# Kernel tuning notes

Hardware: AMD Instinct MI355X
Metric: run time of the kernel (lower is better)

The kernel has to match this reference:

```python
import jax, jax.numpy as jnp
import numpy as np

B = 1024            # batch
F = (16, 16, 16)    # factors (f1, f2, f3)
BOND = 32           # bond dimension
SIZE = 4096         # prod(F)


def setup_inputs() -> dict:
    key = jax.random.key(0)
    k0, k1, k2, k3 = jax.random.split(key, 4)
    x = jax.random.normal(k0, (B, SIZE), dtype=jnp.float32)
    # cores: (r_{k-1}, f_k, f_k, r_k), boundary ranks = 1, init scale 0.01 as in torch
    core0 = jax.random.normal(k1, (1, F[0], F[0], BOND), dtype=jnp.float32) * 0.01
    core1 = jax.random.normal(k2, (BOND, F[1], F[1], BOND), dtype=jnp.float32) * 0.01
    core2 = jax.random.normal(k3, (BOND, F[2], F[2], 1), dtype=jnp.float32) * 0.01
    bias = jnp.zeros((SIZE,), dtype=jnp.float32)
    return {"x": x, "core0": core0, "core1": core1, "core2": core2, "bias": bias}


def reference(x, core0, core1, core2, bias):
    # Batched MPO (tensor-train) matvec: y[b, i1 i2 i3] = sum_{j1 j2 j3, r1 r2}
    #   G0[1, i1, j1, r1] G1[r1, i2, j2, r2] G2[r2, i3, j3, 1] * x[b, j1 j2 j3]
    b = x.shape[0]
    t = x.reshape(b, F[0], F[1], F[2])                       # (B, j1, j2, j3)
    # contract j1 with core0 -> carry bond r, accumulate output index i1 at the end
    t = jnp.einsum('bjkl,aijr->brkli', t, core0)             # (B, r1, j2, j3, i1)
    # contract (r1, j2) with core1
    t = jnp.einsum('brkli,rmks->bslim', t, core1)            # (B, r2, j3, i1, i2)
    # contract (r2, j3) with core2 (right bond t has size 1)
    y = jnp.einsum('bslim,snlt->bimnt', t, core2)            # (B, i1, i2, i3, 1)
    return y.reshape(b, SIZE) + bias
```

## Files before the change

### kernel.cpp

```cpp
#include <hip/hip_runtime.h>
#include <stdint.h>

typedef float f32x4_t __attribute__((ext_vector_type(4)));
typedef __bf16 bf16x8_t __attribute__((ext_vector_type(8)));

#define GLD16(gp, lp) __builtin_amdgcn_global_load_lds( \
    (const __attribute__((address_space(1))) void*)(gp), \
    (__attribute__((address_space(3))) void*)(lp), 16, 0, 0)

__device__ __forceinline__ uint32_t f2bf(float f) {
  uint32_t u = __float_as_uint(f);
  u += 0x7FFFu + ((u >> 16) & 1u);
  return u >> 16;
}
__device__ __forceinline__ uint32_t pack2(float a, float b) {
  return f2bf(a) | (f2bf(b) << 16);
}

__global__ __launch_bounds__(256) void build_w_kernel(
    const float* __restrict__ c0, const float* __restrict__ c1,
    const float* __restrict__ c2, uint16_t* __restrict__ W) {
  __shared__ float M1[16 * 516];
  const int t = threadIdx.x;
  const int bid = blockIdx.x;
  const int i1 = bid >> 4, j1 = bid & 15;

  const float* c0b = c0 + (i1 * 16 + j1) * 32;
  const float4* c1v = (const float4*)c1;
  #pragma unroll 1
  for (int ee = 0; ee < 8; ++ee) {
    const int idx4 = t + 256 * ee;
    float ax = 0.f, ay = 0.f, az = 0.f, aw = 0.f;
    #pragma unroll 8
    for (int r1 = 0; r1 < 32; ++r1) {
      const float g = c0b[r1];
      const float4 v = c1v[r1 * 2048 + idx4];
      ax += g * v.x; ay += g * v.y; az += g * v.z; aw += g * v.w;
    }
    const int idx = idx4 * 4;
    const int i2 = idx >> 9, j2 = (idx >> 5) & 15, r2 = idx & 31;
    float* p = &M1[i2 * 516 + j2 * 32 + r2];
    p[0] = ax; p[1] = ay; p[2] = az; p[3] = aw;
  }
  __syncthreads();

  const int i2 = t >> 4, i3 = t & 15;
  const int irow = (i1 * 16 + i2) * 16 + i3;
  uint16_t* Wr = W + (size_t)irow * 4096 + j1 * 256;
  const float4* c2v = (const float4*)c2;
  const float* M1b = &M1[i2 * 516];

  #pragma unroll 1
  for (int half = 0; half < 2; ++half) {
    float acc[8][16];
    #pragma unroll
    for (int a = 0; a < 8; ++a)
      #pragma unroll
      for (int b = 0; b < 16; ++b) acc[a][b] = 0.f;

    const float* M1h = M1b + half * 8 * 32;
    #pragma unroll 4
    for (int r2 = 0; r2 < 32; ++r2) {
      const float4 q0 = c2v[r2 * 64 + i3 * 4 + 0];
      const float4 q1 = c2v[r2 * 64 + i3 * 4 + 1];
      const float4 q2 = c2v[r2 * 64 + i3 * 4 + 2];
      const float4 q3 = c2v[r2 * 64 + i3 * 4 + 3];
      float gv[16] = {q0.x, q0.y, q0.z, q0.w, q1.x, q1.y, q1.z, q1.w,
                      q2.x, q2.y, q2.z, q2.w, q3.x, q3.y, q3.z, q3.w};
      float m1v[8];
      #pragma unroll
      for (int jj = 0; jj < 8; ++jj) m1v[jj] = M1h[jj * 32 + r2];
      #pragma unroll
      for (int jj = 0; jj < 8; ++jj)
        #pragma unroll
        for (int j3 = 0; j3 < 16; ++j3)
          acc[jj][j3] += m1v[jj] * gv[j3];
    }
    #pragma unroll
    for (int jj = 0; jj < 8; ++jj) {
      uint4 o0, o1;
      o0.x = pack2(acc[jj][0],  acc[jj][1]);  o0.y = pack2(acc[jj][2],  acc[jj][3]);
      o0.z = pack2(acc[jj][4],  acc[jj][5]);  o0.w = pack2(acc[jj][6],  acc[jj][7]);
      o1.x = pack2(acc[jj][8],  acc[jj][9]);  o1.y = pack2(acc[jj][10], acc[jj][11]);
      o1.z = pack2(acc[jj][12], acc[jj][13]); o1.w = pack2(acc[jj][14], acc[jj][15]);
      uint4* dst = (uint4*)(Wr + half * 128 + jj * 16);
      dst[0] = o0; dst[1] = o1;
    }
  }
}

__global__ __launch_bounds__(256) void cvt_x_kernel(const float* __restrict__ x,
                                                    uint32_t* __restrict__ xb) {
  const int i = blockIdx.x * 256 + threadIdx.x;
  const float4* x4 = (const float4*)x;
  const float4 a = x4[2 * i], b = x4[2 * i + 1];
  uint4 o;
  o.x = pack2(a.x, a.y); o.y = pack2(a.z, a.w);
  o.z = pack2(b.x, b.y); o.w = pack2(b.z, b.w);
  ((uint4*)xb)[i] = o;
}

__global__ __launch_bounds__(256, 2) void gemm_bt_bias_kernel(
    const uint16_t* __restrict__ A, const uint16_t* __restrict__ Bt,
    const float* __restrict__ bias, float* __restrict__ C) {
  constexpr int Kd = 4096, Nd = 4096;
  __shared__ uint16_t As[64 * 64];
  __shared__ uint16_t Bs[128 * 64];
  const int t = threadIdx.x;
  const int wid = t >> 6, lane = t & 63;

  const int bid = blockIdx.x;
  const int g = bid & 7, idx = bid >> 3;
  const int ntile = g * 4 + (idx >> 4);
  const int mtile = idx & 15;
  const int brow = mtile * 64, bcol = ntile * 128;

  const uint16_t* Ab = A + (size_t)brow * Kd;
  const uint16_t* Bb = Bt + (size_t)bcol * Kd;

  const int rb = t >> 3;
  const int ce = ((t & 7) * 8) ^ ((rb & 7) << 3);
  const uint16_t* gA = Ab + (size_t)rb * Kd + ce;
  const uint16_t* gB = Bb + (size_t)rb * Kd + ce;
  uint16_t* lA0 = As + wid * 512;
  uint16_t* lA1 = As + 2048 + wid * 512;
  uint16_t* lB0 = Bs + wid * 512;
  uint16_t* lB1 = Bs + 2048 + wid * 512;
  uint16_t* lB2 = Bs + 4096 + wid * 512;
  uint16_t* lB3 = Bs + 6144 + wid * 512;

  const int wm = wid >> 1, wn = wid & 1;
  const int fr = lane & 15, fk = (lane >> 4) * 8;
  const int csw = (fr & 7) << 3;

  f32x4_t zero = {0.f, 0.f, 0.f, 0.f};
  f32x4_t acc[2][4];
  #pragma unroll
  for (int m = 0; m < 2; ++m)
    #pragma unroll
    for (int n = 0; n < 4; ++n) acc[m][n] = zero;

  for (int kt = 0; kt < Kd; kt += 64) {
    GLD16(gA + kt, lA0);
    GLD16(gA + (size_t)32 * Kd + kt, lA1);
    GLD16(gB + kt, lB0);
    GLD16(gB + (size_t)32 * Kd + kt, lB1);
    GLD16(gB + (size_t)64 * Kd + kt, lB2);
    GLD16(gB + (size_t)96 * Kd + kt, lB3);
    __syncthreads();

    bf16x8_t af[2][2], bfr[2][4];
    #pragma unroll
    for (int kk = 0; kk < 2; ++kk) {
      const int col = (kk * 32 + fk) ^ csw;
      #pragma unroll
      for (int m = 0; m < 2; ++m)
        af[kk][m] = *(const bf16x8_t*)(As + (wm * 32 + m * 16 + fr) * 64 + col);
      #pragma unroll
      for (int n = 0; n < 4; ++n)
        bfr[kk][n] = *(const bf16x8_t*)(Bs + (wn * 64 + n * 16 + fr) * 64 + col);
    }
    #pragma unroll
    for (int kk = 0; kk < 2; ++kk)
      #pragma unroll
      for (int m = 0; m < 2; ++m)
        #pragma unroll
        for (int n = 0; n < 4; ++n)
          acc[m][n] = __builtin_amdgcn_mfma_f32_16x16x32_bf16(
              af[kk][m], bfr[kk][n], acc[m][n], 0, 0, 0);
    __syncthreads();
  }

  const int orow = brow + wm * 32 + (lane >> 4) * 4;
  const int ocol = bcol + wn * 64 + fr;
  #pragma unroll
  for (int n = 0; n < 4; ++n) {
    const float bv = bias[ocol + n * 16];
    #pragma unroll
    for (int m = 0; m < 2; ++m) {
      float* Cp = C + (size_t)(orow + m * 16) * Nd + ocol + n * 16;
      #pragma unroll
      for (int r = 0; r < 4; ++r) Cp[(size_t)r * Nd] = acc[m][n][r] + bv;
    }
  }
}

extern "C" void kernel_launch(void* const* d_in, const int* in_sizes, int n_in,
                              void* d_out, int out_size, void* d_ws, size_t ws_size,
                              hipStream_t stream) {
  const float* x    = (const float*)d_in[0];
  const float* c0   = (const float*)d_in[1];
  const float* c1   = (const float*)d_in[2];
  const float* c2   = (const float*)d_in[3];
  const float* bias = (const float*)d_in[4];
  float* y = (float*)d_out;

  uint16_t* W  = (uint16_t*)d_ws;
  uint16_t* xb = (uint16_t*)d_ws + (size_t)4096 * 4096;

  build_w_kernel<<<256, 256, 0, stream>>>(c0, c1, c2, W);
  cvt_x_kernel<<<2048, 256, 0, stream>>>(x, (uint32_t*)xb);
  gemm_bt_bias_kernel<<<512, 256, 0, stream>>>(xb, W, bias, y);
}
```

Measured before the change: 169.9 us.

## Split W construction into two kernels and double-buffer GEMM LDS tiles

The dense W build is split into two stages: one kernel forms the core0·core1 product into an fp32 scratch buffer, and a second, much wider grid contracts it with core2 into bf16 W. This is meant to raise parallelism over the old 256-block kernel, which held a large per-thread accumulator. The GEMM now double-buffers its LDS tiles so the next K-slice load is issued before the current MFMAs, leaving one barrier per iteration. In exchange it doubles LDS use and adds an extra scratch round-trip, with the scratch region reused for xb after build_w2 finishes.

```diff
diff --git a/kernel.cpp b/kernel.cpp
--- a/kernel.cpp
+++ b/kernel.cpp
@@ -17,76 +17,78 @@
   return f2bf(a) | (f2bf(b) << 16);
 }
 
-__global__ __launch_bounds__(256) void build_w_kernel(
+__global__ __launch_bounds__(256) void build_m01_kernel(
     const float* __restrict__ c0, const float* __restrict__ c1,
-    const float* __restrict__ c2, uint16_t* __restrict__ W) {
-  __shared__ float M1[16 * 516];
-  const int t = threadIdx.x;
+    float* __restrict__ M01) {
+  const int a = blockIdx.x, t = threadIdx.x;
+  const int i1 = a >> 4, i2 = a & 15, j1 = t >> 4, j2 = t & 15;
+  const float* c0p = c0 + (i1 * 16 + j1) * 32;
+  const float4* c1v = (const float4*)(c1 + i2 * 512 + j2 * 32);
+
+  float acc[32];
+  #pragma unroll
+  for (int r2 = 0; r2 < 32; ++r2) acc[r2] = 0.f;
+
+  #pragma unroll 4
+  for (int r1 = 0; r1 < 32; ++r1) {
+    const float g = c0p[r1];
+    #pragma unroll
+    for (int q = 0; q < 8; ++q) {
+      const float4 v = c1v[r1 * 2048 + q];
+      acc[q * 4 + 0] += g * v.x; acc[q * 4 + 1] += g * v.y;
+      acc[q * 4 + 2] += g * v.z; acc[q * 4 + 3] += g * v.w;
+    }
+  }
+  float4* dst = (float4*)(M01 + (size_t)a * 8192 + t * 32);
+  #pragma unroll
+  for (int q = 0; q < 8; ++q) {
+    float4 v = {acc[q * 4 + 0], acc[q * 4 + 1], acc[q * 4 + 2], acc[q * 4 + 3]};
+    dst[q] = v;
+  }
+}
+
+__global__ __launch_bounds__(256) void build_w2_kernel(
+    const float* __restrict__ M01, const float* __restrict__ c2,
+    uint16_t* __restrict__ W) {
+  __shared__ float C2L[32 * 16];
   const int bid = blockIdx.x;
-  const int i1 = bid >> 4, j1 = bid & 15;
-
-  const float* c0b = c0 + (i1 * 16 + j1) * 32;
-  const float4* c1v = (const float4*)c1;
-  #pragma unroll 1
-  for (int ee = 0; ee < 8; ++ee) {
-    const int idx4 = t + 256 * ee;
-    float ax = 0.f, ay = 0.f, az = 0.f, aw = 0.f;
-    #pragma unroll 8
-    for (int r1 = 0; r1 < 32; ++r1) {
-      const float g = c0b[r1];
-      const float4 v = c1v[r1 * 2048 + idx4];
-      ax += g * v.x; ay += g * v.y; az += g * v.z; aw += g * v.w;
-    }
-    const int idx = idx4 * 4;
-    const int i2 = idx >> 9, j2 = (idx >> 5) & 15, r2 = idx & 31;
-    float* p = &M1[i2 * 516 + j2 * 32 + r2];
-    p[0] = ax; p[1] = ay; p[2] = az; p[3] = aw;
+  const int a = bid >> 4, i3 = bid & 15, t = threadIdx.x;
+
+  if (t < 128) {
+    ((float4*)C2L)[t] = ((const float4*)c2)[(t >> 2) * 64 + i3 * 4 + (t & 3)];
   }
   __syncthreads();
 
-  const int i2 = t >> 4, i3 = t & 15;
-  const int irow = (i1 * 16 + i2) * 16 + i3;
-  uint16_t* Wr = W + (size_t)irow * 4096 + j1 * 256;
-  const float4* c2v = (const float4*)c2;
-  const float* M1b = &M1[i2 * 516];
-
-  #pragma unroll 1
-  for (int half = 0; half < 2; ++half) {
-    float acc[8][16];
-    #pragma unroll
-    for (int a = 0; a < 8; ++a)
-      #pragma unroll
-      for (int b = 0; b < 16; ++b) acc[a][b] = 0.f;
-
-    const float* M1h = M1b + half * 8 * 32;
-    #pragma unroll 4
-    for (int r2 = 0; r2 < 32; ++r2) {
-      const float4 q0 = c2v[r2 * 64 + i3 * 4 + 0];
-      const float4 q1 = c2v[r2 * 64 + i3 * 4 + 1];
-      const float4 q2 = c2v[r2 * 64 + i3 * 4 + 2];
-      const float4 q3 = c2v[r2 * 64 + i3 * 4 + 3];
-      float gv[16] = {q0.x, q0.y, q0.z, q0.w, q1.x, q1.y, q1.z, q1.w,
-                      q2.x, q2.y, q2.z, q2.w, q3.x, q3.y, q3.z, q3.w};
-      float m1v[8];
-      #pragma unroll
-      for (int jj = 0; jj < 8; ++jj) m1v[jj] = M1h[jj * 32 + r2];
-      #pragma unroll
-      for (int jj = 0; jj < 8; ++jj)
-        #pragma unroll
-        for (int j3 = 0; j3 < 16; ++j3)
-          acc[jj][j3] += m1v[jj] * gv[j3];
-    }
-    #pragma unroll
-    for (int jj = 0; jj < 8; ++jj) {
-      uint4 o0, o1;
-      o0.x = pack2(acc[jj][0],  acc[jj][1]);  o0.y = pack2(acc[jj][2],  acc[jj][3]);
-      o0.z = pack2(acc[jj][4],  acc[jj][5]);  o0.w = pack2(acc[jj][6],  acc[jj][7]);
-      o1.x = pack2(acc[jj][8],  acc[jj][9]);  o1.y = pack2(acc[jj][10], acc[jj][11]);
-      o1.z = pack2(acc[jj][12], acc[jj][13]); o1.w = pack2(acc[jj][14], acc[jj][15]);
-      uint4* dst = (uint4*)(Wr + half * 128 + jj * 16);
-      dst[0] = o0; dst[1] = o1;
-    }
-  }
+  float M[32];
+  const float4* mp = (const float4*)(M01 + (size_t)a * 8192 + t * 32);
+  #pragma unroll
+  for (int q = 0; q < 8; ++q) {
+    const float4 v = mp[q];
+    M[q * 4 + 0] = v.x; M[q * 4 + 1] = v.y; M[q * 4 + 2] = v.z; M[q * 4 + 3] = v.w;
+  }
+
+  float acc[16];
+  #pragma unroll
+  for (int j = 0; j < 16; ++j) acc[j] = 0.f;
+
+  #pragma unroll 4
+  for (int r2 = 0; r2 < 32; ++r2) {
+    const float4* cp = (const float4*)(C2L + r2 * 16);
+    const float4 q0 = cp[0], q1 = cp[1], q2 = cp[2], q3 = cp[3];
+    const float m = M[r2];
+    acc[0]  += m * q0.x; acc[1]  += m * q0.y; acc[2]  += m * q0.z; acc[3]  += m * q0.w;
+    acc[4]  += m * q1.x; acc[5]  += m * q1.y; acc[6]  += m * q1.z; acc[7]  += m * q1.w;
+    acc[8]  += m * q2.x; acc[9]  += m * q2.y; acc[10] += m * q2.z; acc[11] += m * q2.w;
+    acc[12] += m * q3.x; acc[13] += m * q3.y; acc[14] += m * q3.z; acc[15] += m * q3.w;
+  }
+
+  uint4 o0, o1;
+  o0.x = pack2(acc[0],  acc[1]);  o0.y = pack2(acc[2],  acc[3]);
+  o0.z = pack2(acc[4],  acc[5]);  o0.w = pack2(acc[6],  acc[7]);
+  o1.x = pack2(acc[8],  acc[9]);  o1.y = pack2(acc[10], acc[11]);
+  o1.z = pack2(acc[12], acc[13]); o1.w = pack2(acc[14], acc[15]);
+  uint4* dst = (uint4*)(W + (size_t)(a * 16 + i3) * 4096 + t * 16);
+  dst[0] = o0; dst[1] = o1;
 }
 
 __global__ __launch_bounds__(256) void cvt_x_kernel(const float* __restrict__ x,
@@ -104,8 +106,8 @@
     const uint16_t* __restrict__ A, const uint16_t* __restrict__ Bt,
     const float* __restrict__ bias, float* __restrict__ C) {
   constexpr int Kd = 4096, Nd = 4096;
-  __shared__ uint16_t As[64 * 64];
-  __shared__ uint16_t Bs[128 * 64];
+  __shared__ uint16_t As[2][64 * 64];
+  __shared__ uint16_t Bs[2][128 * 64];
   const int t = threadIdx.x;
   const int wid = t >> 6, lane = t & 63;
 
@@ -122,12 +124,7 @@
   const int ce = ((t & 7) * 8) ^ ((rb & 7) << 3);
   const uint16_t* gA = Ab + (size_t)rb * Kd + ce;
   const uint16_t* gB = Bb + (size_t)rb * Kd + ce;
-  uint16_t* lA0 = As + wid * 512;
-  uint16_t* lA1 = As + 2048 + wid * 512;
-  uint16_t* lB0 = Bs + wid * 512;
-  uint16_t* lB1 = Bs + 2048 + wid * 512;
-  uint16_t* lB2 = Bs + 4096 + wid * 512;
-  uint16_t* lB3 = Bs + 6144 + wid * 512;
+  const int wofs = wid * 512;
 
   const int wm = wid >> 1, wn = wid & 1;
   const int fr = lane & 15, fk = (lane >> 4) * 8;
@@ -140,14 +137,22 @@
     #pragma unroll
     for (int n = 0; n < 4; ++n) acc[m][n] = zero;
 
+  #define STAGE(buf, kt)                                             \
+    do {                                                             \
+      GLD16(gA + (kt), As[buf] + wofs);                              \
+      GLD16(gA + (size_t)32 * Kd + (kt), As[buf] + 2048 + wofs);     \
+      GLD16(gB + (kt), Bs[buf] + wofs);                              \
+      GLD16(gB + (size_t)32 * Kd + (kt), Bs[buf] + 2048 + wofs);     \
+      GLD16(gB + (size_t)64 * Kd + (kt), Bs[buf] + 4096 + wofs);     \
+      GLD16(gB + (size_t)96 * Kd + (kt), Bs[buf] + 6144 + wofs);     \
+    } while (0)
+
+  STAGE(0, 0);
+  __syncthreads();
+
+  int cur = 0;
   for (int kt = 0; kt < Kd; kt += 64) {
-    GLD16(gA + kt, lA0);
-    GLD16(gA + (size_t)32 * Kd + kt, lA1);
-    GLD16(gB + kt, lB0);
-    GLD16(gB + (size_t)32 * Kd + kt, lB1);
-    GLD16(gB + (size_t)64 * Kd + kt, lB2);
-    GLD16(gB + (size_t)96 * Kd + kt, lB3);
-    __syncthreads();
+    if (kt + 64 < Kd) STAGE(cur ^ 1, kt + 64);
 
     bf16x8_t af[2][2], bfr[2][4];
     #pragma unroll
@@ -155,10 +160,10 @@
       const int col = (kk * 32 + fk) ^ csw;
       #pragma unroll
       for (int m = 0; m < 2; ++m)
-        af[kk][m] = *(const bf16x8_t*)(As + (wm * 32 + m * 16 + fr) * 64 + col);
+        af[kk][m] = *(const bf16x8_t*)(As[cur] + (wm * 32 + m * 16 + fr) * 64 + col);
       #pragma unroll
       for (int n = 0; n < 4; ++n)
-        bfr[kk][n] = *(const bf16x8_t*)(Bs + (wn * 64 + n * 16 + fr) * 64 + col);
+        bfr[kk][n] = *(const bf16x8_t*)(Bs[cur] + (wn * 64 + n * 16 + fr) * 64 + col);
     }
     #pragma unroll
     for (int kk = 0; kk < 2; ++kk)
@@ -168,8 +173,11 @@
         for (int n = 0; n < 4; ++n)
           acc[m][n] = __builtin_amdgcn_mfma_f32_16x16x32_bf16(
               af[kk][m], bfr[kk][n], acc[m][n], 0, 0, 0);
+
     __syncthreads();
-  }
+    cur ^= 1;
+  }
+  #undef STAGE
 
   const int orow = brow + wm * 32 + (lane >> 4) * 4;
   const int ocol = bcol + wn * 64 + fr;
@@ -195,10 +203,13 @@
   const float* bias = (const float*)d_in[4];
   float* y = (float*)d_out;
 
-  uint16_t* W  = (uint16_t*)d_ws;
-  uint16_t* xb = (uint16_t*)d_ws + (size_t)4096 * 4096;
-
-  build_w_kernel<<<256, 256, 0, stream>>>(c0, c1, c2, W);
+  uint16_t* W   = (uint16_t*)d_ws;
+  char*     slab = (char*)d_ws + (size_t)4096 * 4096 * 2;
+  float*    M01 = (float*)slab;
+  uint16_t* xb  = (uint16_t*)slab;
+
+  build_m01_kernel<<<256, 256, 0, stream>>>(c0, c1, M01);
+  build_w2_kernel<<<4096, 256, 0, stream>>>(M01, c2, W);
   cvt_x_kernel<<<2048, 256, 0, stream>>>(x, (uint32_t*)xb);
   gemm_bt_bias_kernel<<<512, 256, 0, stream>>>(xb, W, bias, y);
 }
```

New measurement: 192.0 us. 13.0% more time.
